# Optimization experiments

Hardware: AMD Instinct MI355X
Metric: run time of the kernel (lower is better)

Reference implementation:

```python
import jax, jax.numpy as jnp
import numpy as np

K = 5  # kernel size (kernel_size=[5])


def setup_inputs() -> dict:
    key = jax.random.key(0)
    k1, k2 = jax.random.split(key)
    B, C, H, W = 4, 64, 128, 128
    data = jax.random.normal(k1, (B, C, H, W), dtype=jnp.float32)
    core = jax.random.normal(k2, (B, K * K * C, H, W), dtype=jnp.float32) * 0.1
    return {"data": data, "core": core}


def reference(data, core):
    # data: [B, C, H, W]; core: [B, K^2*C, H, W] -> viewed as [B, K^2, C, H, W]
    B, C, H, W = data.shape
    core = core.reshape(B, K * K, C, H, W)
    pad = K // 2
    dp = jnp.pad(data, ((0, 0), (0, 0), (pad, pad), (pad, pad)))
    # feature_stack[:, i*K+j] = dp[..., i:i+H, j:j+W]  (same shift order as torch loop)
    stack = jnp.stack(
        [dp[:, :, i:i + H, j:j + W] for i in range(K) for j in range(K)], axis=1
    )  # [B, K^2, C, H, W]
    # per-pixel dynamic conv: elementwise multiply with predicted kernels, sum over K^2
    return jnp.sum(core * stack, axis=1)  # [B, C, H, W]
```

## Files before the change

kernel.cpp:

```cpp
#include <hip/hip_runtime.h>

#define KK 5
#define NB 4
#define NC 64
#define NH 128
#define NW 128
#define W4 (NW / 4)
#define HW (NH * NW)
#define CHW (NC * HW)

__global__ __launch_bounds__(256) void kconv_kernel(const float* __restrict__ data,
                                                    const float* __restrict__ core,
                                                    float* __restrict__ out) {
    int tid = blockIdx.x * blockDim.x + threadIdx.x;
    int w4 = tid & (W4 - 1);
    int h  = (tid >> 5) & (NH - 1);
    int c  = (tid >> 12) & (NC - 1);
    int b  = tid >> 18;

    int wbase = w4 << 2;

    const float* dbase = data + (size_t)(b * NC + c) * HW;
    const float* cbase = core + (size_t)(b * KK * KK + 0) * (size_t)CHW
                              + (size_t)c * HW + h * NW + wbase;

    float4 acc = make_float4(0.f, 0.f, 0.f, 0.f);

    #pragma unroll
    for (int i = 0; i < KK; ++i) {
        int hh = h + i - 2;
        float d[8];
        bool row_ok = (hh >= 0) && (hh < NH);
        const float* row = dbase + hh * NW + (wbase - 2);
        #pragma unroll
        for (int t = 0; t < 8; ++t) {
            int col = wbase - 2 + t;
            bool ok = row_ok && (col >= 0) && (col < NW);
            d[t] = ok ? row[t] : 0.f;
        }
        #pragma unroll
        for (int j = 0; j < KK; ++j) {
            int k = i * KK + j;
            const float4 ck = *reinterpret_cast<const float4*>(cbase + (size_t)k * CHW);
            acc.x = fmaf(ck.x, d[j + 0], acc.x);
            acc.y = fmaf(ck.y, d[j + 1], acc.y);
            acc.z = fmaf(ck.z, d[j + 2], acc.z);
            acc.w = fmaf(ck.w, d[j + 3], acc.w);
        }
    }

    float4* op = reinterpret_cast<float4*>(out + (size_t)(b * NC + c) * HW + h * NW + wbase);
    *op = acc;
}

extern "C" void kernel_launch(void* const* d_in, const int* in_sizes, int n_in,
                              void* d_out, int out_size, void* d_ws, size_t ws_size,
                              hipStream_t stream) {
    const float* data = (const float*)d_in[0];
    const float* core = (const float*)d_in[1];
    float* out = (float*)d_out;

    int total_threads = NB * NC * NH * W4;
    dim3 block(256);
    dim3 grid(total_threads / 256);
    kconv_kernel<<<grid, block, 0, stream>>>(data, core, out);
}
```

Before: 549.2 us.

## Stage data tile in LDS and use nontemporal loads for core stream

Each block now loads a padded 12x132 data tile for one (b,c) and 8 rows into shared memory, then computes outputs from LDS instead of issuing many unaligned, bounds-checked global loads per thread. The large per-pixel kernel tensor is read with nontemporal loads and the output written with nontemporal stores to avoid polluting caches. This adds a barrier and an LDS fill phase per block, and an occupancy hint in launch bounds.

```diff
diff --git a/kernel.cpp b/kernel.cpp
--- a/kernel.cpp
+++ b/kernel.cpp
@@ -5,43 +5,62 @@
 #define NC 64
 #define NH 128
 #define NW 128
-#define W4 (NW / 4)
 #define HW (NH * NW)
 #define CHW (NC * HW)
+#define RPB 8
+#define LROWS (RPB + 4)
+#define LW 132
 
-__global__ __launch_bounds__(256) void kconv_kernel(const float* __restrict__ data,
-                                                    const float* __restrict__ core,
-                                                    float* __restrict__ out) {
-    int tid = blockIdx.x * blockDim.x + threadIdx.x;
-    int w4 = tid & (W4 - 1);
-    int h  = (tid >> 5) & (NH - 1);
-    int c  = (tid >> 12) & (NC - 1);
-    int b  = tid >> 18;
+typedef float vfloat4 __attribute__((ext_vector_type(4)));
 
-    int wbase = w4 << 2;
+__global__ __launch_bounds__(256, 4) void kconv_kernel(const float* __restrict__ data,
+                                                       const float* __restrict__ core,
+                                                       float* __restrict__ out) {
+    __shared__ float sdata[LROWS][LW];
+
+    const int tid = threadIdx.x;
+    const int blk = blockIdx.x;
+    const int hblk = blk & (NH / RPB - 1);
+    const int c    = (blk >> 4) & (NC - 1);
+    const int b    = blk >> 10;
+    const int h0   = hblk * RPB;
 
     const float* dbase = data + (size_t)(b * NC + c) * HW;
-    const float* cbase = core + (size_t)(b * KK * KK + 0) * (size_t)CHW
-                              + (size_t)c * HW + h * NW + wbase;
 
-    float4 acc = make_float4(0.f, 0.f, 0.f, 0.f);
+    #pragma unroll
+    for (int idx = tid; idx < LROWS * LW; idx += 256) {
+        int r   = idx / LW;
+        int col = idx - r * LW;
+        int gh  = h0 + r - 2;
+        int gw  = col - 2;
+        float v = 0.f;
+        if (gh >= 0 && gh < NH && gw >= 0 && gw < NW)
+            v = dbase[gh * NW + gw];
+        sdata[r][col] = v;
+    }
+    __syncthreads();
+
+    const int w4    = tid & 31;
+    const int hr    = tid >> 5;
+    const int h     = h0 + hr;
+    const int wbase = w4 << 2;
+
+    const float* cbase = core + (size_t)b * (KK * KK) * (size_t)CHW
+                              + (size_t)c * HW + (size_t)(h * NW + wbase);
+
+    vfloat4 acc = {0.f, 0.f, 0.f, 0.f};
 
     #pragma unroll
     for (int i = 0; i < KK; ++i) {
-        int hh = h + i - 2;
-        float d[8];
-        bool row_ok = (hh >= 0) && (hh < NH);
-        const float* row = dbase + hh * NW + (wbase - 2);
-        #pragma unroll
-        for (int t = 0; t < 8; ++t) {
-            int col = wbase - 2 + t;
-            bool ok = row_ok && (col >= 0) && (col < NW);
-            d[t] = ok ? row[t] : 0.f;
-        }
+        const float* lrow = &sdata[hr + i][wbase];
+        vfloat4 d0 = *reinterpret_cast<const vfloat4*>(lrow);
+        vfloat4 d1 = *reinterpret_cast<const vfloat4*>(lrow + 4);
+        float d[8] = {d0.x, d0.y, d0.z, d0.w, d1.x, d1.y, d1.z, d1.w};
         #pragma unroll
         for (int j = 0; j < KK; ++j) {
-            int k = i * KK + j;
-            const float4 ck = *reinterpret_cast<const float4*>(cbase + (size_t)k * CHW);
+            const int k = i * KK + j;
+            vfloat4 ck = __builtin_nontemporal_load(
+                reinterpret_cast<const vfloat4*>(cbase + (size_t)k * CHW));
             acc.x = fmaf(ck.x, d[j + 0], acc.x);
             acc.y = fmaf(ck.y, d[j + 1], acc.y);
             acc.z = fmaf(ck.z, d[j + 2], acc.z);
@@ -49,8 +68,9 @@
         }
     }
 
-    float4* op = reinterpret_cast<float4*>(out + (size_t)(b * NC + c) * HW + h * NW + wbase);
-    *op = acc;
+    vfloat4* op = reinterpret_cast<vfloat4*>(out + (size_t)(b * NC + c) * HW
+                                                 + (size_t)(h * NW + wbase));
+    __builtin_nontemporal_store(acc, op);
 }
 
 extern "C" void kernel_launch(void* const* d_in, const int* in_sizes, int n_in,
@@ -60,8 +80,7 @@
     const float* core = (const float*)d_in[1];
     float* out = (float*)d_out;
 
-    int total_threads = NB * NC * NH * W4;
     dim3 block(256);
-    dim3 grid(total_threads / 256);
+    dim3 grid(NB * NC * (NH / RPB));
     kconv_kernel<<<grid, block, 0, stream>>>(data, core, out);
 }
```

New measurement: 546.1 us. About the same (-0.6%).
